# Performance work log

Hardware: AMD Instinct MI355X
Metric: run time of the kernel (lower is better)

## Reference

```python
import jax, jax.numpy as jnp
import numpy as np

RADIUS = 0.1
NSAMPLE = 32
STRIDE = 4
EPS = 1e-5


def fps(p, M):
    # Furthest point sampling. p: [B, N, 3] -> idx [B, M] int32. First point is index 0.
    B, N, _ = p.shape

    def body(carry, _):
        dmin, last = carry
        lp = jnp.take_along_axis(p, last[:, None, None], axis=1)  # [B,1,3]
        d = jnp.sum((p - lp) ** 2, axis=-1)                       # [B,N]
        dmin = jnp.minimum(dmin, d)
        nxt = jnp.argmax(dmin, axis=-1).astype(jnp.int32)
        return (dmin, nxt), nxt

    first = jnp.zeros((B,), jnp.int32)
    dmin0 = jnp.full((B, N), jnp.inf, p.dtype)
    _, rest = jax.lax.scan(body, (dmin0, first), None, length=M - 1)
    return jnp.concatenate([first[None, :], rest], axis=0).T  # [B,M]


def ball_query(new_p, p, radius, K):
    # For each query, first K support indices with dist < radius (CUDA ballquery semantics:
    # pad with first found index; 0 if none). new_p [B,M,3], p [B,N,3] -> [B,M,K] int32.
    N = p.shape[1]
    d2 = (jnp.sum(new_p ** 2, -1)[:, :, None] + jnp.sum(p ** 2, -1)[:, None, :]
          - 2.0 * jnp.einsum('bmd,bnd->bmn', new_p, p))  # [B,M,N]
    scores = jnp.where(d2 < radius * radius,
                       jnp.arange(N, dtype=jnp.int32)[None, None, :], N)
    neg_vals, _ = jax.lax.top_k(-scores, K)  # K smallest scores, ascending
    idx = -neg_vals
    first = jnp.where(idx[..., :1] >= N, 0, idx[..., :1])
    return jnp.where(idx >= N, first, idx)


def bn(x, g, b):
    # BatchNorm (training-mode batch stats) over all dims except channel dim 1.
    axes = tuple(i for i in range(x.ndim) if i != 1)
    m = jnp.mean(x, axes, keepdims=True)
    v = jnp.var(x, axes, keepdims=True)
    shape = (1, -1) + (1,) * (x.ndim - 2)
    return g.reshape(shape) * (x - m) * jax.lax.rsqrt(v + EPS) + b.reshape(shape)


def setup_inputs() -> dict:
    key = jax.random.key(0)
    ks = jax.random.split(key, 6)
    B, N, C = 4, 8192, 64
    return {
        'p': jax.random.uniform(ks[0], (B, N, 3), jnp.float32),
        'f': jax.random.normal(ks[1], (B, C, N), jnp.float32),
        'w1': jax.random.normal(ks[2], (64, 3 + C), jnp.float32) * 0.05,
        'g1': jnp.ones((64,), jnp.float32),
        'b1': jnp.zeros((64,), jnp.float32),
        'w2': jax.random.normal(ks[3], (128, 64), jnp.float32) * 0.05,
        'g2': jnp.ones((128,), jnp.float32),
        'b2': jnp.zeros((128,), jnp.float32),
        'w_skip': jax.random.normal(ks[4], (128, C), jnp.float32) * 0.05,
        'b_skip': jnp.zeros((128,), jnp.float32),
    }


def reference(p, f, w1, g1, b1, w2, g2, b2, w_skip, b_skip):
    B, N, _ = p.shape
    C = f.shape[1]
    M = N // STRIDE
    idx = fps(p, M)                                                # [B,M]
    new_p = jnp.take_along_axis(p, idx[:, :, None], axis=1)        # [B,M,3]
    # residual branch: gather sampled features, 1x1 conv1d skip
    fi = jnp.take_along_axis(f, jnp.broadcast_to(idx[:, None, :], (B, C, M)), axis=2)
    identity = jnp.einsum('oc,bcm->bom', w_skip, fi) + b_skip[None, :, None]
    # ball-query grouping
    nidx = ball_query(new_p, p, RADIUS, NSAMPLE)                   # [B,M,K]
    flat = nidx.reshape(B, 1, M * NSAMPLE)
    pj = jnp.take_along_axis(p.transpose(0, 2, 1),
                             jnp.broadcast_to(flat, (B, 3, M * NSAMPLE)),
                             axis=2).reshape(B, 3, M, NSAMPLE)
    dp = pj - new_p.transpose(0, 2, 1)[:, :, :, None]              # [B,3,M,K]
    fj = jnp.take_along_axis(f, jnp.broadcast_to(flat, (B, C, M * NSAMPLE)),
                             axis=2).reshape(B, C, M, NSAMPLE)
    x = jnp.concatenate([dp, fj], axis=1)                          # [B,3+C,M,K]
    # conv-bn-relu, conv-bn (last block no act because use_res)
    x = jax.nn.relu(bn(jnp.einsum('oc,bcmk->bomk', w1, x), g1, b1))
    x = bn(jnp.einsum('oc,bcmk->bomk', w2, x), g2, b2)
    fout = jnp.max(x, axis=-1)                                     # [B,128,M]
    fout = jax.nn.relu(fout + identity)
    return new_p, fout, idx
```

## Files before the change

### kernel.cpp

```cpp
#include <hip/hip_runtime.h>
#include <math.h>

#define BB 4
#define NP 8192
#define CF 64
#define MQ 2048
#define KS 32

#define WS_G      0u
#define WS_NIDX   2097152u
#define WS_IDXI   2359296u
#define WS_ST1    2367488u
#define WS_ST2    2375680u
#define WS_SC1    2392064u
#define WS_SC2    2392192u
#define WS_MAXY2  2392448u

typedef float v2f __attribute__((ext_vector_type(2)));

#define FPS_T 256
#define FPS_NK 16

template <int CTRL>
__device__ __forceinline__ unsigned long long dpp_max_step(unsigned long long k) {
  int lo = (int)(unsigned)k;
  int hi = (int)(unsigned)(k >> 32);
  int slo = __builtin_amdgcn_update_dpp(0, lo, CTRL, 0xF, 0xF, true);
  int shi = __builtin_amdgcn_update_dpp(0, hi, CTRL, 0xF, 0xF, true);
  unsigned long long s =
      ((unsigned long long)(unsigned)shi << 32) | (unsigned long long)(unsigned)slo;
  return s > k ? s : k;
}

__global__ __launch_bounds__(256, 1) void fps_fused_kernel(
    const float* __restrict__ p, float* __restrict__ out, int* __restrict__ idx_i,
    const float* __restrict__ f, float* __restrict__ gout,
    const float* __restrict__ w1) {
#pragma clang fp contract(off)
  __shared__ __align__(16) char smem[NP * 16 + MQ * 4 + 2 * 4 * 8];
  int bx = blockIdx.x;
  int t = threadIdx.x;

  if (bx >= 4) {
    float (*tile)[65] = (float (*)[65])smem;
    float (*wlds)[68] = (float (*)[68])(smem + 16640);
    float* plds = (float*)(smem + 16640 + 17408);
    int tb = bx - 4;
    int b = tb >> 7;
    int n0 = (tb & 127) * 64;
    int cc = t >> 6;
    int nn = t & 63;
    #pragma unroll
    for (int r = 0; r < 16; ++r) {
      int c = cc * 16 + r;
      tile[c][nn] = f[((size_t)b * 64 + c) * NP + n0 + nn];
    }
    for (int i = t; i < 64 * 67; i += 256) {
      wlds[i / 67][i % 67] = w1[i];
    }
    if (t < 192) plds[t] = p[((size_t)b * NP + n0) * 3 + t];
    __syncthreads();
    int wv = t >> 6, lane = t & 63;
    float wreg[67];
    #pragma unroll
    for (int c = 0; c < 67; ++c) wreg[c] = wlds[lane][c];
    for (int q = 0; q < 16; ++q) {
      int pt = wv * 16 + q;
      float acc = wreg[0] * plds[pt * 3 + 0];
      acc += wreg[1] * plds[pt * 3 + 1];
      acc += wreg[2] * plds[pt * 3 + 2];
      #pragma unroll
      for (int c = 0; c < 64; ++c) acc += wreg[3 + c] * tile[c][pt];
      gout[((size_t)b * NP + n0 + pt) * 64 + lane] = acc;
    }
    return;
  }

  float4* sp4 = (float4*)smem;
  int* win = (int*)(smem + NP * 16);
  unsigned long long* wkey = (unsigned long long*)(smem + NP * 16 + MQ * 4);

  int b = bx;
  const float* pb = p + (size_t)b * NP * 3;
  float* out_newp = out;
  float* out_idxf = out + BB*MQ*3 + (size_t)BB*128*MQ;

  v2f px2[FPS_NK], py2[FPS_NK], pz2[FPS_NK];
  float dmn0[FPS_NK], dmn1[FPS_NK];
  #pragma unroll
  for (int k = 0; k < FPS_NK; ++k) {
    int i0 = (2*k) * FPS_T + t;
    int i1 = i0 + FPS_T;
    float x0 = pb[i0*3+0], y0 = pb[i0*3+1], z0 = pb[i0*3+2];
    float x1 = pb[i1*3+0], y1 = pb[i1*3+1], z1 = pb[i1*3+2];
    px2[k] = (v2f){x0, x1}; py2[k] = (v2f){y0, y1}; pz2[k] = (v2f){z0, z1};
    sp4[i0] = make_float4(x0, y0, z0, 0.0f);
    sp4[i1] = make_float4(x1, y1, z1, 0.0f);
    dmn0[k] = INFINITY; dmn1[k] = INFINITY;
  }
  if (t == 0) win[0] = 0;
  __syncthreads();
  float lx = sp4[0].x, ly = sp4[0].y, lz = sp4[0].z;
  unsigned nt = ~(unsigned)t;

  for (int j = 1; j < MQ; ++j) {
#pragma clang fp contract(off)
    v2f l2x = (v2f){lx, lx}, l2y = (v2f){ly, ly}, l2z = (v2f){lz, lz};
    float bv0 = -1.0f, bv1 = -1.0f;
    unsigned bk0 = 0u, bk1 = 0u;
    #pragma unroll
    for (int k = 0; k < FPS_NK; ++k) {
      v2f dx = px2[k] - l2x;
      v2f dy = py2[k] - l2y;
      v2f dz = pz2[k] - l2z;
      v2f dd = ((dx*dx) + (dy*dy)) + (dz*dz);
      float m0 = fminf(dmn0[k], dd.x);  dmn0[k] = m0;
      float m1 = fminf(dmn1[k], dd.y);  dmn1[k] = m1;
      bool g0 = m0 > bv0;
      bv0 = g0 ? m0 : bv0;
      bk0 = g0 ? (unsigned)k : bk0;
      bool g1 = m1 > bv1;
      bv1 = g1 ? m1 : bv1;
      bk1 = g1 ? (unsigned)k : bk1;
    }
    unsigned bn0 = nt - (bk0 << 9);
    unsigned bn1 = nt - (bk1 << 9) - 256u;
    unsigned long long k0 =
        ((unsigned long long)__float_as_uint(bv0) << 32) | (unsigned long long)bn0;
    unsigned long long k1 =
        ((unsigned long long)__float_as_uint(bv1) << 32) | (unsigned long long)bn1;
    unsigned long long key = k0 > k1 ? k0 : k1;
    key = dpp_max_step<0x111>(key);
    key = dpp_max_step<0x112>(key);
    key = dpp_max_step<0x114>(key);
    key = dpp_max_step<0x118>(key);
    key = dpp_max_step<0x142>(key);
    key = dpp_max_step<0x143>(key);
    if ((t & 63) == 63) wkey[(j & 1) * 4 + (t >> 6)] = key;
    __syncthreads();
    const ulonglong2* wk2 = (const ulonglong2*)(&wkey[(j & 1) * 4]);
    ulonglong2 ka = wk2[0];
    ulonglong2 kb = wk2[1];
    unsigned long long m0 = ka.x > ka.y ? ka.x : ka.y;
    unsigned long long m1 = kb.x > kb.y ? kb.x : kb.y;
    unsigned long long kw = m0 > m1 ? m0 : m1;
    int wi = (int)(~(unsigned)kw);
    float4 c = sp4[wi];
    lx = c.x; ly = c.y; lz = c.z;
    if (t == 0) win[j] = wi;
  }

  __syncthreads();
  #pragma unroll
  for (int k = 0; k < MQ / FPS_T; ++k) {
    int j = k * FPS_T + t;
    int wi = win[j];
    out_idxf[b*MQ + j] = (float)wi;
    idx_i[b*MQ + j] = wi;
    float4 c = sp4[wi];
    float* np_ = &out_newp[(size_t)(b*MQ + j) * 3];
    np_[0] = c.x; np_[1] = c.y; np_[2] = c.z;
  }
}

__global__ __launch_bounds__(256) void ballq_kernel(
    const float* __restrict__ p, const float* __restrict__ newp,
    int* __restrict__ nidx) {
  int qid = blockIdx.x * 4 + (threadIdx.x >> 6);
  int lane = threadIdx.x & 63;
  int b = qid >> 11;
  const float* pb = p + (size_t)b * NP * 3;
  float qx = newp[qid*3], qy = newp[qid*3+1], qz = newp[qid*3+2];
  float sq_q = __fadd_rn(__fadd_rn(__fmul_rn(qx,qx), __fmul_rn(qy,qy)), __fmul_rn(qz,qz));
  const float R2 = (float)(0.1 * 0.1);
  int found = 0, first = -1;
  int* outp = nidx + (size_t)qid * KS;
  for (int base = 0; base < NP; base += 64) {
    int n = base + lane;
    float x = pb[n*3], y = pb[n*3+1], z = pb[n*3+2];
    float sq_p = __fadd_rn(__fadd_rn(__fmul_rn(x,x), __fmul_rn(y,y)), __fmul_rn(z,z));
    float dot  = __fadd_rn(__fadd_rn(__fmul_rn(qx,x), __fmul_rn(qy,y)), __fmul_rn(qz,z));
    float d2   = __fadd_rn(__fadd_rn(sq_q, sq_p), __fmul_rn(-2.0f, dot));
    bool hit = d2 < R2;
    unsigned long long mask = __ballot(hit);
    if (mask) {
      if (first < 0) first = base + __builtin_ctzll(mask);
      int cnt = __popcll(mask);
      if (found < KS) {
        int rank = __popcll(mask & ((1ull << lane) - 1ull));
        if (hit && found + rank < KS) outp[found + rank] = n;
      }
      found += cnt;
      if (found >= KS) break;
    }
  }
  int fcl = found < KS ? found : KS;
  int padv = first < 0 ? 0 : first;
  if (lane >= fcl && lane < KS) outp[lane] = padv;
}

__global__ __launch_bounds__(256) void p1_kernel(
    const float* __restrict__ g, const float* __restrict__ newp,
    const float* __restrict__ w1, const int* __restrict__ nidx,
    float* __restrict__ stats1) {
  __shared__ float wbs[4][64], wbq[4][64];
  int wv = threadIdx.x >> 6, lane = threadIdx.x & 63;
  int qid = blockIdx.x * 4 + wv;
  int b = qid >> 11;
  int nv = (lane < KS) ? nidx[(size_t)qid * KS + lane] : 0;
  float qx = newp[qid*3], qy = newp[qid*3+1], qz = newp[qid*3+2];
  float w0 = w1[lane*67+0], w1c = w1[lane*67+1], w2c = w1[lane*67+2];
  float hq = w0*qx + w1c*qy + w2c*qz;
  float ss = 0.f, qq = 0.f;
  for (int kb = 0; kb < KS; kb += 8) {
    float gv[8];
    #pragma unroll
    for (int u = 0; u < 8; ++u) {
      int n = __shfl(nv, kb + u);
      gv[u] = g[((size_t)b * NP + n) * 64 + lane];
    }
    #pragma unroll
    for (int u = 0; u < 8; ++u) {
      float a = gv[u] - hq;
      ss += a; qq += a * a;
    }
  }
  wbs[wv][lane] = ss; wbq[wv][lane] = qq;
  __syncthreads();
  if (threadIdx.x < 64) {
    float s  = wbs[0][threadIdx.x] + wbs[1][threadIdx.x] + wbs[2][threadIdx.x] + wbs[3][threadIdx.x];
    float s2 = wbq[0][threadIdx.x] + wbq[1][threadIdx.x] + wbq[2][threadIdx.x] + wbq[3][threadIdx.x];
    int slice = blockIdx.x & 63;
    atomicAdd(&stats1[(slice*2+0)*64 + threadIdx.x], s);
    atomicAdd(&stats1[(slice*2+1)*64 + threadIdx.x], s2);
  }
}

__global__ void fin1_kernel(const float* __restrict__ stats1,
                            const float* __restrict__ g, const float* __restrict__ bb,
                            float* __restrict__ sc) {
  int o = threadIdx.x;
  float s = 0.f, q = 0.f;
  for (int sl = 0; sl < 64; ++sl) { s += stats1[(sl*2+0)*64+o]; q += stats1[(sl*2+1)*64+o]; }
  const float cnt = (float)(BB * MQ * KS);
  float mean = s / cnt;
  float var = q / cnt - mean * mean;
  float rstd = 1.0f / sqrtf(var + 1e-5f);
  float gs = g[o] * rstd;
  sc[o] = gs;
  sc[64+o] = bb[o] - mean * gs;
}

__global__ void fin2_kernel(const float* __restrict__ stats2,
                            const float* __restrict__ g, const float* __restrict__ bb,
                            float* __restrict__ sc) {
  int o = threadIdx.x;
  float s = 0.f, q = 0.f;
  for (int sl = 0; sl < 64; ++sl) { s += stats2[(sl*2+0)*128+o]; q += stats2[(sl*2+1)*128+o]; }
  const float cnt = (float)(BB * MQ * KS);
  float mean = s / cnt;
  float var = q / cnt - mean * mean;
  float rstd = 1.0f / sqrtf(var + 1e-5f);
  float gs = g[o] * rstd;
  sc[o] = gs;
  sc[128+o] = bb[o] - mean * gs;
}

__global__ __launch_bounds__(256) void p2_kernel(
    const float* __restrict__ g, const float* __restrict__ newp,
    const float* __restrict__ w1, const float* __restrict__ w2,
    const int* __restrict__ nidx, const float* __restrict__ sc1,
    float* __restrict__ stats2, float* __restrict__ maxy2) {
  __shared__ __align__(16) float xbuf[4][KS][68];
  __shared__ float wbs[4][128], wbq[4][128];
  int wv = threadIdx.x >> 6, lane = threadIdx.x & 63;
  int qid = blockIdx.x * 4 + wv;
  int b = qid >> 11;
  int nv = (lane < KS) ? nidx[(size_t)qid * KS + lane] : 0;
  float qx = newp[qid*3], qy = newp[qid*3+1], qz = newp[qid*3+2];
  float w0 = w1[lane*67+0], w1c = w1[lane*67+1], w2c = w1[lane*67+2];
  float hq = w0*qx + w1c*qy + w2c*qz;
  float s1v = sc1[lane], t1v = sc1[64 + lane];
  for (int kb = 0; kb < KS; kb += 8) {
    float gv[8];
    #pragma unroll
    for (int u = 0; u < 8; ++u) {
      int n = __shfl(nv, kb + u);
      gv[u] = g[((size_t)b * NP + n) * 64 + lane];
    }
    #pragma unroll
    for (int u = 0; u < 8; ++u) {
      float a = gv[u] - hq;
      float h = fmaxf(0.0f, fmaf(a, s1v, t1v));
      xbuf[wv][kb + u][lane] = h;
    }
  }
  __syncthreads();
  const float4* w2a = (const float4*)(w2 + (size_t)lane * 64);
  const float4* w2b = (const float4*)(w2 + (size_t)(lane + 64) * 64);
  float4 wra[16], wrb[16];
  #pragma unroll
  for (int c4 = 0; c4 < 16; ++c4) { wra[c4] = w2a[c4]; wrb[c4] = w2b[c4]; }
  float ss0 = 0.f, qq0 = 0.f, mx0 = -INFINITY;
  float ss1 = 0.f, qq1 = 0.f, mx1 = -INFINITY;
  for (int kk = 0; kk < KS; ++kk) {
    const float4* hr = (const float4*)(&xbuf[wv][kk][0]);
    float a0 = 0.f, a1 = 0.f;
    #pragma unroll
    for (int c4 = 0; c4 < 16; ++c4) {
      float4 h4 = hr[c4];
      float4 wa = wra[c4]; float4 wb = wrb[c4];
      a0 += wa.x*h4.x + wa.y*h4.y + wa.z*h4.z + wa.w*h4.w;
      a1 += wb.x*h4.x + wb.y*h4.y + wb.z*h4.z + wb.w*h4.w;
    }
    ss0 += a0; qq0 += a0*a0; mx0 = fmaxf(mx0, a0);
    ss1 += a1; qq1 += a1*a1; mx1 = fmaxf(mx1, a1);
  }
  maxy2[(size_t)qid * 128 + lane] = mx0;
  maxy2[(size_t)qid * 128 + 64 + lane] = mx1;
  wbs[wv][lane] = ss0; wbs[wv][64+lane] = ss1;
  wbq[wv][lane] = qq0; wbq[wv][64+lane] = qq1;
  __syncthreads();
  if (threadIdx.x < 128) {
    float s  = wbs[0][threadIdx.x] + wbs[1][threadIdx.x] + wbs[2][threadIdx.x] + wbs[3][threadIdx.x];
    float s2 = wbq[0][threadIdx.x] + wbq[1][threadIdx.x] + wbq[2][threadIdx.x] + wbq[3][threadIdx.x];
    int slice = blockIdx.x & 63;
    atomicAdd(&stats2[(slice*2+0)*128 + threadIdx.x], s);
    atomicAdd(&stats2[(slice*2+1)*128 + threadIdx.x], s2);
  }
}

__global__ __launch_bounds__(256) void p3_kernel(
    const float* __restrict__ f, const int* __restrict__ idx_i,
    const float* __restrict__ w_skip, const float* __restrict__ b_skip,
    const float* __restrict__ sc2, const float* __restrict__ maxy2,
    float* __restrict__ outf) {
  __shared__ __align__(16) float flds[4][64];
  int wv = threadIdx.x >> 6, lane = threadIdx.x & 63;
  int qid = blockIdx.x * 4 + wv;
  int b = qid >> 11, m = qid & (MQ - 1);
  int n = idx_i[qid];
  flds[wv][lane] = f[((size_t)b * 64 + lane) * NP + n];
  const float4* f4 = (const float4*)(&flds[wv][0]);
  const float4* wa = (const float4*)(w_skip + (size_t)lane * 64);
  const float4* wb = (const float4*)(w_skip + (size_t)(lane + 64) * 64);
  float a0 = b_skip[lane], a1 = b_skip[lane + 64];
  #pragma unroll
  for (int c4 = 0; c4 < 16; ++c4) {
    float4 x = f4[c4]; float4 u = wa[c4]; float4 v = wb[c4];
    a0 += u.x*x.x + u.y*x.y + u.z*x.z + u.w*x.w;
    a1 += v.x*x.x + v.y*x.y + v.z*x.z + v.w*x.w;
  }
  float v0 = maxy2[(size_t)qid * 128 + lane];
  float v1 = maxy2[(size_t)qid * 128 + 64 + lane];
  float r0 = fmaxf(0.0f, fmaf(v0, sc2[lane],      sc2[128 + lane])      + a0);
  float r1 = fmaxf(0.0f, fmaf(v1, sc2[lane + 64], sc2[128 + lane + 64]) + a1);
  outf[((size_t)b * 128 + lane) * MQ + m] = r0;
  outf[((size_t)b * 128 + lane + 64) * MQ + m] = r1;
}

extern "C" void kernel_launch(void* const* d_in, const int* in_sizes, int n_in,
                              void* d_out, int out_size, void* d_ws, size_t ws_size,
                              hipStream_t stream) {
  (void)in_sizes; (void)n_in; (void)out_size; (void)ws_size;
  const float* p   = (const float*)d_in[0];
  const float* f   = (const float*)d_in[1];
  const float* w1  = (const float*)d_in[2];
  const float* g1  = (const float*)d_in[3];
  const float* b1  = (const float*)d_in[4];
  const float* w2  = (const float*)d_in[5];
  const float* g2  = (const float*)d_in[6];
  const float* b2  = (const float*)d_in[7];
  const float* wsk = (const float*)d_in[8];
  const float* bsk = (const float*)d_in[9];
  float* out = (float*)d_out;
  float* wsf = (float*)d_ws;

  float* gbuf  = wsf + WS_G;
  int*   nidx  = (int*)(wsf + WS_NIDX);
  int*   idxi  = (int*)(wsf + WS_IDXI);
  float* st1   = wsf + WS_ST1;
  float* st2   = wsf + WS_ST2;
  float* sc1   = wsf + WS_SC1;
  float* sc2   = wsf + WS_SC2;
  float* maxy2 = wsf + WS_MAXY2;

  float* out_newp = out;
  float* out_f    = out + BB*MQ*3;

  (void)hipMemsetAsync(st1, 0, (8192 + 16384) * sizeof(float), stream);

  fps_fused_kernel<<<4 + 512, FPS_T, 0, stream>>>(p, out, idxi, f, gbuf, w1);
  ballq_kernel<<<BB*MQ/4, 256, 0, stream>>>(p, out_newp, nidx);
  p1_kernel<<<BB*MQ/4, 256, 0, stream>>>(gbuf, out_newp, w1, nidx, st1);
  fin1_kernel<<<1, 64, 0, stream>>>(st1, g1, b1, sc1);
  p2_kernel<<<BB*MQ/4, 256, 0, stream>>>(gbuf, out_newp, w1, w2, nidx, sc1, st2, maxy2);
  fin2_kernel<<<1, 128, 0, stream>>>(st2, g2, b2, sc2);
  p3_kernel<<<BB*MQ/4, 256, 0, stream>>>(f, idxi, wsk, bsk, sc2, maxy2, out_f);
}
```

Before: 1.906 ms.

## Fuse ball query with BN1 stats pass and inline BN finalize kernels

New measurement: 1.932 ms. About the same (+1.3%).

```diff
diff --git a/kernel.cpp b/kernel.cpp
--- a/kernel.cpp
+++ b/kernel.cpp
@@ -12,8 +12,6 @@
 #define WS_IDXI   2359296u
 #define WS_ST1    2367488u
 #define WS_ST2    2375680u
-#define WS_SC1    2392064u
-#define WS_SC2    2392192u
 #define WS_MAXY2  2392448u
 
 typedef float v2f __attribute__((ext_vector_type(2)));
@@ -43,8 +41,8 @@
 
   if (bx >= 4) {
     float (*tile)[65] = (float (*)[65])smem;
-    float (*wlds)[68] = (float (*)[68])(smem + 16640);
-    float* plds = (float*)(smem + 16640 + 17408);
+    float (*wlds)[69] = (float (*)[69])(smem + 16640);
+    float* plds = (float*)(smem + 16640 + 17664);
     int tb = bx - 4;
     int b = tb >> 7;
     int n0 = (tb & 127) * 64;
@@ -163,21 +161,25 @@
   }
 }
 
-__global__ __launch_bounds__(256) void ballq_kernel(
+__global__ __launch_bounds__(256) void bp1_kernel(
     const float* __restrict__ p, const float* __restrict__ newp,
-    int* __restrict__ nidx) {
-  int qid = blockIdx.x * 4 + (threadIdx.x >> 6);
-  int lane = threadIdx.x & 63;
+    const float* __restrict__ g, const float* __restrict__ w1,
+    int* __restrict__ nidx, float* __restrict__ stats1) {
+  __shared__ int nvbuf[4][KS];
+  __shared__ float wbs[4][64], wbq[4][64];
+  int wv = threadIdx.x >> 6, lane = threadIdx.x & 63;
+  int qid = blockIdx.x * 4 + wv;
   int b = qid >> 11;
   const float* pb = p + (size_t)b * NP * 3;
   float qx = newp[qid*3], qy = newp[qid*3+1], qz = newp[qid*3+2];
   float sq_q = __fadd_rn(__fadd_rn(__fmul_rn(qx,qx), __fmul_rn(qy,qy)), __fmul_rn(qz,qz));
   const float R2 = (float)(0.1 * 0.1);
   int found = 0, first = -1;
-  int* outp = nidx + (size_t)qid * KS;
+  float x = pb[lane*3], y = pb[lane*3+1], z = pb[lane*3+2];
   for (int base = 0; base < NP; base += 64) {
+    int nf = (base + 64 < NP) ? (base + 64 + lane) : lane;
+    float xn = pb[nf*3], yn = pb[nf*3+1], zn = pb[nf*3+2];
     int n = base + lane;
-    float x = pb[n*3], y = pb[n*3+1], z = pb[n*3+2];
     float sq_p = __fadd_rn(__fadd_rn(__fmul_rn(x,x), __fmul_rn(y,y)), __fmul_rn(z,z));
     float dot  = __fadd_rn(__fadd_rn(__fmul_rn(qx,x), __fmul_rn(qy,y)), __fmul_rn(qz,z));
     float d2   = __fadd_rn(__fadd_rn(sq_q, sq_p), __fmul_rn(-2.0f, dot));
@@ -188,27 +190,17 @@
       int cnt = __popcll(mask);
       if (found < KS) {
         int rank = __popcll(mask & ((1ull << lane) - 1ull));
-        if (hit && found + rank < KS) outp[found + rank] = n;
+        if (hit && found + rank < KS) nvbuf[wv][found + rank] = n;
       }
       found += cnt;
       if (found >= KS) break;
     }
+    x = xn; y = yn; z = zn;
   }
   int fcl = found < KS ? found : KS;
   int padv = first < 0 ? 0 : first;
-  if (lane >= fcl && lane < KS) outp[lane] = padv;
-}
-
-__global__ __launch_bounds__(256) void p1_kernel(
-    const float* __restrict__ g, const float* __restrict__ newp,
-    const float* __restrict__ w1, const int* __restrict__ nidx,
-    float* __restrict__ stats1) {
-  __shared__ float wbs[4][64], wbq[4][64];
-  int wv = threadIdx.x >> 6, lane = threadIdx.x & 63;
-  int qid = blockIdx.x * 4 + wv;
-  int b = qid >> 11;
-  int nv = (lane < KS) ? nidx[(size_t)qid * KS + lane] : 0;
-  float qx = newp[qid*3], qy = newp[qid*3+1], qz = newp[qid*3+2];
+  if (lane >= fcl && lane < KS) nvbuf[wv][lane] = padv;
+  if (lane < KS) nidx[(size_t)qid * KS + lane] = nvbuf[wv][lane];
   float w0 = w1[lane*67+0], w1c = w1[lane*67+1], w2c = w1[lane*67+2];
   float hq = w0*qx + w1c*qy + w2c*qz;
   float ss = 0.f, qq = 0.f;
@@ -216,7 +208,7 @@
     float gv[8];
     #pragma unroll
     for (int u = 0; u < 8; ++u) {
-      int n = __shfl(nv, kb + u);
+      int n = nvbuf[wv][kb + u];
       gv[u] = g[((size_t)b * NP + n) * 64 + lane];
     }
     #pragma unroll
@@ -236,51 +228,35 @@
   }
 }
 
-__global__ void fin1_kernel(const float* __restrict__ stats1,
-                            const float* __restrict__ g, const float* __restrict__ bb,
-                            float* __restrict__ sc) {
-  int o = threadIdx.x;
-  float s = 0.f, q = 0.f;
-  for (int sl = 0; sl < 64; ++sl) { s += stats1[(sl*2+0)*64+o]; q += stats1[(sl*2+1)*64+o]; }
-  const float cnt = (float)(BB * MQ * KS);
-  float mean = s / cnt;
-  float var = q / cnt - mean * mean;
-  float rstd = 1.0f / sqrtf(var + 1e-5f);
-  float gs = g[o] * rstd;
-  sc[o] = gs;
-  sc[64+o] = bb[o] - mean * gs;
-}
-
-__global__ void fin2_kernel(const float* __restrict__ stats2,
-                            const float* __restrict__ g, const float* __restrict__ bb,
-                            float* __restrict__ sc) {
-  int o = threadIdx.x;
-  float s = 0.f, q = 0.f;
-  for (int sl = 0; sl < 64; ++sl) { s += stats2[(sl*2+0)*128+o]; q += stats2[(sl*2+1)*128+o]; }
-  const float cnt = (float)(BB * MQ * KS);
-  float mean = s / cnt;
-  float var = q / cnt - mean * mean;
-  float rstd = 1.0f / sqrtf(var + 1e-5f);
-  float gs = g[o] * rstd;
-  sc[o] = gs;
-  sc[128+o] = bb[o] - mean * gs;
-}
-
 __global__ __launch_bounds__(256) void p2_kernel(
     const float* __restrict__ g, const float* __restrict__ newp,
     const float* __restrict__ w1, const float* __restrict__ w2,
-    const int* __restrict__ nidx, const float* __restrict__ sc1,
+    const int* __restrict__ nidx, const float* __restrict__ stats1,
+    const float* __restrict__ g1, const float* __restrict__ b1,
     float* __restrict__ stats2, float* __restrict__ maxy2) {
   __shared__ __align__(16) float xbuf[4][KS][68];
   __shared__ float wbs[4][128], wbq[4][128];
   int wv = threadIdx.x >> 6, lane = threadIdx.x & 63;
   int qid = blockIdx.x * 4 + wv;
   int b = qid >> 11;
+  float s1v, t1v;
+  {
+    float s = 0.f, q = 0.f;
+    for (int sl = 0; sl < 64; ++sl) {
+      s += stats1[(sl*2+0)*64 + lane];
+      q += stats1[(sl*2+1)*64 + lane];
+    }
+    const float cnt = (float)(BB * MQ * KS);
+    float mean = s / cnt;
+    float var = q / cnt - mean * mean;
+    float rstd = 1.0f / sqrtf(var + 1e-5f);
+    s1v = g1[lane] * rstd;
+    t1v = b1[lane] - mean * s1v;
+  }
   int nv = (lane < KS) ? nidx[(size_t)qid * KS + lane] : 0;
   float qx = newp[qid*3], qy = newp[qid*3+1], qz = newp[qid*3+2];
   float w0 = w1[lane*67+0], w1c = w1[lane*67+1], w2c = w1[lane*67+2];
   float hq = w0*qx + w1c*qy + w2c*qz;
-  float s1v = sc1[lane], t1v = sc1[64 + lane];
   for (int kb = 0; kb < KS; kb += 8) {
     float gv[8];
     #pragma unroll
@@ -333,13 +309,35 @@
 __global__ __launch_bounds__(256) void p3_kernel(
     const float* __restrict__ f, const int* __restrict__ idx_i,
     const float* __restrict__ w_skip, const float* __restrict__ b_skip,
-    const float* __restrict__ sc2, const float* __restrict__ maxy2,
-    float* __restrict__ outf) {
+    const float* __restrict__ stats2,
+    const float* __restrict__ g2, const float* __restrict__ b2,
+    const float* __restrict__ maxy2, float* __restrict__ outf) {
   __shared__ __align__(16) float flds[4][64];
   int wv = threadIdx.x >> 6, lane = threadIdx.x & 63;
   int qid = blockIdx.x * 4 + wv;
   int b = qid >> 11, m = qid & (MQ - 1);
   int n = idx_i[qid];
+  float sc0, sh0, sc1v, sh1;
+  {
+    float s0 = 0.f, q0 = 0.f, s1 = 0.f, q1 = 0.f;
+    for (int sl = 0; sl < 64; ++sl) {
+      s0 += stats2[(sl*2+0)*128 + lane];
+      q0 += stats2[(sl*2+1)*128 + lane];
+      s1 += stats2[(sl*2+0)*128 + lane + 64];
+      q1 += stats2[(sl*2+1)*128 + lane + 64];
+    }
+    const float cnt = (float)(BB * MQ * KS);
+    float mean0 = s0 / cnt;
+    float var0 = q0 / cnt - mean0 * mean0;
+    float rstd0 = 1.0f / sqrtf(var0 + 1e-5f);
+    sc0 = g2[lane] * rstd0;
+    sh0 = b2[lane] - mean0 * sc0;
+    float mean1 = s1 / cnt;
+    float var1 = q1 / cnt - mean1 * mean1;
+    float rstd1 = 1.0f / sqrtf(var1 + 1e-5f);
+    sc1v = g2[lane + 64] * rstd1;
+    sh1 = b2[lane + 64] - mean1 * sc1v;
+  }
   flds[wv][lane] = f[((size_t)b * 64 + lane) * NP + n];
   const float4* f4 = (const float4*)(&flds[wv][0]);
   const float4* wa = (const float4*)(w_skip + (size_t)lane * 64);
@@ -353,8 +351,8 @@
   }
   float v0 = maxy2[(size_t)qid * 128 + lane];
   float v1 = maxy2[(size_t)qid * 128 + 64 + lane];
-  float r0 = fmaxf(0.0f, fmaf(v0, sc2[lane],      sc2[128 + lane])      + a0);
-  float r1 = fmaxf(0.0f, fmaf(v1, sc2[lane + 64], sc2[128 + lane + 64]) + a1);
+  float r0 = fmaxf(0.0f, fmaf(v0, sc0,  sh0) + a0);
+  float r1 = fmaxf(0.0f, fmaf(v1, sc1v, sh1) + a1);
   outf[((size_t)b * 128 + lane) * MQ + m] = r0;
   outf[((size_t)b * 128 + lane + 64) * MQ + m] = r1;
 }
@@ -381,8 +379,6 @@
   int*   idxi  = (int*)(wsf + WS_IDXI);
   float* st1   = wsf + WS_ST1;
   float* st2   = wsf + WS_ST2;
-  float* sc1   = wsf + WS_SC1;
-  float* sc2   = wsf + WS_SC2;
   float* maxy2 = wsf + WS_MAXY2;
 
   float* out_newp = out;
@@ -391,10 +387,7 @@
   (void)hipMemsetAsync(st1, 0, (8192 + 16384) * sizeof(float), stream);
 
   fps_fused_kernel<<<4 + 512, FPS_T, 0, stream>>>(p, out, idxi, f, gbuf, w1);
-  ballq_kernel<<<BB*MQ/4, 256, 0, stream>>>(p, out_newp, nidx);
-  p1_kernel<<<BB*MQ/4, 256, 0, stream>>>(gbuf, out_newp, w1, nidx, st1);
-  fin1_kernel<<<1, 64, 0, stream>>>(st1, g1, b1, sc1);
-  p2_kernel<<<BB*MQ/4, 256, 0, stream>>>(gbuf, out_newp, w1, w2, nidx, sc1, st2, maxy2);
-  fin2_kernel<<<1, 128, 0, stream>>>(st2, g2, b2, sc2);
-  p3_kernel<<<BB*MQ/4, 256, 0, stream>>>(f, idxi, wsk, bsk, sc2, maxy2, out_f);
-}
+  bp1_kernel<<<BB*MQ/4, 256, 0, stream>>>(p, out_newp, gbuf, w1, nidx, st1);
+  p2_kernel<<<BB*MQ/4, 256, 0, stream>>>(gbuf, out_newp, w1, w2, nidx, st1, g1, b1, st2, maxy2);
+  p3_kernel<<<BB*MQ/4, 256, 0, stream>>>(f, idxi, wsk, bsk, st2, g2, b2, maxy2, out_f);
+}
```
